# Kernel optimization log

Measured on AMD Instinct MI355X. Metric: run time of the kernel, lower is better.

Reference implementation:

```python
import jax, jax.numpy as jnp
import numpy as np

B, N, C, H = 16, 4096, 256, 4
D = C // H


def setup_inputs() -> dict:
    key = jax.random.key(0)
    ks = jax.random.split(key, 16)
    s = 0.02
    inp = {
        "x": jax.random.normal(ks[0], (B, N, C), jnp.float32),
        "encoding": jax.random.normal(ks[1], (2, B, 1, N, D), jnp.float32),
        "Wqkv_w": jax.random.normal(ks[2], (3 * C, C), jnp.float32) * s,
        "Wqkv_b": jnp.zeros((3 * C,), jnp.float32),
        "tssa_qkv_w": jax.random.normal(ks[3], (C, C), jnp.float32) * s,
        "tssa_qkv_b": jnp.zeros((C,), jnp.float32),
        "temp": jnp.ones((H, 1), jnp.float32),
        "tssa_out_w": jax.random.normal(ks[4], (C, C), jnp.float32) * s,
        "tssa_out_b": jnp.zeros((C,), jnp.float32),
        "out_proj_w": jax.random.normal(ks[5], (C, C), jnp.float32) * s,
        "out_proj_b": jnp.zeros((C,), jnp.float32),
        "ffn1_w": jax.random.normal(ks[6], (2 * C, 2 * C), jnp.float32) * s,
        "ffn1_b": jnp.zeros((2 * C,), jnp.float32),
        "ln_g": jnp.ones((2 * C,), jnp.float32),
        "ln_b": jnp.zeros((2 * C,), jnp.float32),
        "ffn2_w": jax.random.normal(ks[7], (C, 2 * C), jnp.float32) * s,
        "ffn2_b": jnp.zeros((C,), jnp.float32),
    }
    return inp


def _rotate_half(t):
    # (..., d) -> pairwise rotate: (x1, x2) -> (-x2, x1)
    t2 = t.reshape(t.shape[:-1] + (-1, 2))
    x1, x2 = t2[..., 0], t2[..., 1]
    return jnp.stack((-x2, x1), axis=-1).reshape(t.shape)


def reference(x, encoding, Wqkv_w, Wqkv_b, tssa_qkv_w, tssa_qkv_b, temp,
              tssa_out_w, tssa_out_b, out_proj_w, out_proj_b,
              ffn1_w, ffn1_b, ln_g, ln_b, ffn2_w, ffn2_b):
    b, n, c = x.shape
    h, d = H, D
    # QKV projection, layout (h, d, 3) on last dim as in unflatten(-1,(h,-1,3))
    qkv = (x @ Wqkv_w.T + Wqkv_b).reshape(b, n, h, d, 3).transpose(0, 2, 1, 3, 4)  # b h n d 3
    q, k, v = qkv[..., 0], qkv[..., 1], qkv[..., 2]
    rope = lambda t: t * encoding[0] + _rotate_half(t) * encoding[1]
    q = rope(q)
    k = rope(k)
    flat = lambda t: t.transpose(0, 2, 1, 3).reshape(b, n, c)  # b h n d -> b n (h d)
    w_input = (flat(q) + flat(k) + flat(v)) / 3.0
    # TSSA attention
    w = (w_input @ tssa_qkv_w.T + tssa_qkv_b).reshape(b, n, h, d).transpose(0, 2, 1, 3)  # b h n d
    norm = jnp.sqrt(jnp.sum(w * w, axis=2, keepdims=True))  # L2 over sequence axis N
    w_normed = w / jnp.maximum(norm, 1e-12)
    sum_ws = jnp.sum(w_normed * w_normed, axis=-1)  # b h n
    Pi = jax.nn.softmax(sum_ws * temp[None, :, :], axis=1)  # softmax over heads
    Pi_norm = Pi / (jnp.sum(Pi, axis=-1, keepdims=True) + 1e-8)
    dots = jnp.einsum('bhn,bhnd->bh', Pi_norm, w * w)  # (b,h,1,d) summed over d
    attn = 1.0 / (1.0 + dots)  # b h
    out = -(w * Pi[..., None]) * attn[:, :, None, None]  # b h n d
    out = out.transpose(0, 2, 1, 3).reshape(b, n, c)
    context = out @ tssa_out_w.T + tssa_out_b
    message = context @ out_proj_w.T + out_proj_b
    # residual FFN
    cat = jnp.concatenate([x, message], axis=-1)  # b n 2c
    h1 = cat @ ffn1_w.T + ffn1_b
    mu = jnp.mean(h1, axis=-1, keepdims=True)
    var = jnp.mean((h1 - mu) ** 2, axis=-1, keepdims=True)
    ln = (h1 - mu) / jnp.sqrt(var + 1e-5) * ln_g + ln_b
    g = jax.nn.gelu(ln, approximate=False)
    return x + (g @ ffn2_w.T + ffn2_b)
```

## Files before the change

### kernel.cpp

```cpp
#include <hip/hip_runtime.h>
#include <math.h>

#define Bc 16
#define Nc 4096

typedef __attribute__((ext_vector_type(8))) short short8;
typedef __attribute__((ext_vector_type(4))) float floatx4;

__device__ __forceinline__ unsigned short f2bf(float f) {
    union { float f; unsigned int u; } v; v.f = f;
    unsigned int u = v.u;
    return (unsigned short)((u + 0x7fffu + ((u >> 16) & 1u)) >> 16);
}
__device__ __forceinline__ float bf2f(unsigned short u) {
    union { unsigned int u; float f; } v; v.u = ((unsigned int)u) << 16;
    return v.f;
}

__device__ __forceinline__ void gll16(const unsigned short* g, unsigned short* l) {
    __builtin_amdgcn_global_load_lds(
        (const __attribute__((address_space(1))) void*)g,
        (__attribute__((address_space(3))) void*)l,
        16, 0, 0);
}

template <int EPI, typename TOUT>
__global__ __launch_bounds__(512) void gemm_bf(
    const unsigned short* __restrict__ A0, int lda0,
    const unsigned short* __restrict__ A1, int lda1, int K0,
    const unsigned short* __restrict__ W,
    const float* __restrict__ bias,
    const unsigned short* __restrict__ resid_bf,
    const float* __restrict__ Pi,
    const float* __restrict__ Sb,
    const float* __restrict__ Tb,
    const float* __restrict__ enc,
    float* __restrict__ norm2,
    float* __restrict__ rowstats,
    TOUT* __restrict__ C, int N, int K)
{
    __shared__ alignas(16) unsigned short As[128 * 64];
    __shared__ alignas(16) unsigned short Bs[256 * 64];

    const int t = threadIdx.x;
    const int bn = blockIdx.x, bm = blockIdx.y;
    const int lane = t & 63, wave = t >> 6;
    const int wm = wave >> 2, wn = wave & 3;
    const int quad = lane >> 4, l16 = lane & 15;
    const int rt = t >> 3, st = t & 7;

    floatx4 acc[4][4];
    #pragma unroll
    for (int i = 0; i < 4; ++i)
        #pragma unroll
        for (int j = 0; j < 4; ++j)
            acc[i][j] = (floatx4){0.f, 0.f, 0.f, 0.f};

    for (int k0 = 0; k0 < K; k0 += 64) {
        #pragma unroll
        for (int hh = 0; hh < 2; ++hh) {
            const int row = hh * 64 + rt;
            const int col = k0 + (st ^ (row & 7)) * 8;
            unsigned short* ldsa = As + row * 64 + st * 8;
            const size_t grow = (size_t)bm * 128 + row;
            if constexpr (EPI == 2) {
                const int b = (int)(grow >> 12);
                const int hd = col >> 6;
                const float s = Sb[b * 4 + hd] + 1e-8f;
                const float at = s / (s + Tb[b * 4 + hd]);
                const float sc = -Pi[grow * 4 + hd] * at;
                const short8 a = *(const short8*)(A0 + grow * (size_t)lda0 + col);
                short8 o;
                #pragma unroll
                for (int j = 0; j < 8; ++j) o[j] = (short)f2bf(bf2f((unsigned short)a[j]) * sc);
                *(short8*)ldsa = o;
            } else {
                const unsigned short* src = (col < K0)
                    ? (A0 + grow * (size_t)lda0 + col)
                    : (A1 + grow * (size_t)lda1 + (col - K0));
                gll16(src, ldsa);
            }
        }
        #pragma unroll
        for (int hh = 0; hh < 4; ++hh) {
            const int row = hh * 64 + rt;
            const int col = k0 + (st ^ (row & 7)) * 8;
            gll16(W + ((size_t)bn * 256 + row) * (size_t)K + col, Bs + row * 64 + st * 8);
        }
        __syncthreads();
        #pragma unroll
        for (int kk = 0; kk < 2; ++kk) {
            short8 af[4], wf[4];
            #pragma unroll
            for (int i = 0; i < 4; ++i) {
                const int ra = wm * 64 + i * 16 + l16;
                af[i] = *(const short8*)(As + ra * 64 + ((quad + kk * 4) ^ (ra & 7)) * 8);
                const int rw = wn * 64 + i * 16 + l16;
                wf[i] = *(const short8*)(Bs + rw * 64 + ((quad + kk * 4) ^ (rw & 7)) * 8);
            }
            #pragma unroll
            for (int mi = 0; mi < 4; ++mi)
                #pragma unroll
                for (int ni = 0; ni < 4; ++ni)
                    acc[mi][ni] = __builtin_amdgcn_mfma_f32_16x16x32_bf16(
                        wf[ni], af[mi], acc[mi][ni], 0, 0, 0);
        }
        __syncthreads();
    }

    float rs[4], rq[4];
    if constexpr (EPI == 4) {
        #pragma unroll
        for (int m = 0; m < 4; ++m) { rs[m] = 0.f; rq[m] = 0.f; }
    }

    #pragma unroll
    for (int mi = 0; mi < 4; ++mi) {
        const size_t row = (size_t)bm * 128 + wm * 64 + mi * 16 + l16;
        #pragma unroll
        for (int ni = 0; ni < 4; ++ni) {
            const int cb = bn * 256 + wn * 64 + ni * 16 + quad * 4;
            const float4 b4 = *(const float4*)(bias + cb);
            if constexpr (EPI == 5) {
                const int j = cb >> 2;
                const int h = j >> 5, d = (j & 31) * 2;
                const float s0 = acc[mi][ni][0] + b4.x;
                const float s1 = acc[mi][ni][1] + b4.y;
                const float v0 = acc[mi][ni][2] + b4.z;
                const float v1 = acc[mi][ni][3] + b4.w;
                const float2 e0 = *(const float2*)(enc + row * 64 + d);
                const float2 e1 = *(const float2*)(enc + 4194304 + row * 64 + d);
                const float r0 = s0 * e0.x - s1 * e1.x;
                const float r1 = s1 * e0.y + s0 * e1.y;
                ushort2 o;
                o.x = f2bf((r0 + v0) * (1.f / 3.f));
                o.y = f2bf((r1 + v1) * (1.f / 3.f));
                *(ushort2*)((unsigned short*)C + row * 256 + h * 64 + d) = o;
                continue;
            }
            float v[4] = {acc[mi][ni][0] + b4.x, acc[mi][ni][1] + b4.y,
                          acc[mi][ni][2] + b4.z, acc[mi][ni][3] + b4.w};
            if constexpr (EPI == 3) {
                const ushort4 xr = *(const ushort4*)(resid_bf + row * (size_t)N + cb);
                v[0] += bf2f(xr.x); v[1] += bf2f(xr.y);
                v[2] += bf2f(xr.z); v[3] += bf2f(xr.w);
            }
            if constexpr (EPI == 4) {
                #pragma unroll
                for (int rg = 0; rg < 4; ++rg) { rs[mi] += v[rg]; rq[mi] += v[rg] * v[rg]; }
            }
            if constexpr (EPI == 1) {
                #pragma unroll
                for (int rg = 0; rg < 4; ++rg) {
                    float s = v[rg] * v[rg];
                    s += __shfl_xor(s, 1, 64);
                    s += __shfl_xor(s, 2, 64);
                    s += __shfl_xor(s, 4, 64);
                    s += __shfl_xor(s, 8, 64);
                    if (l16 == 0) atomicAdd(&norm2[(bm >> 5) * 256 + cb + rg], s);
                }
            }
            if constexpr (__is_same(TOUT, float)) {
                float4 o; o.x = v[0]; o.y = v[1]; o.z = v[2]; o.w = v[3];
                *(float4*)(C + row * (size_t)N + cb) = o;
            } else {
                ushort4 o;
                o.x = f2bf(v[0]); o.y = f2bf(v[1]); o.z = f2bf(v[2]); o.w = f2bf(v[3]);
                *(ushort4*)(C + row * (size_t)N + cb) = o;
            }
        }
    }
    if constexpr (EPI == 4) {
        #pragma unroll
        for (int mi = 0; mi < 4; ++mi) {
            float s = rs[mi], q = rq[mi];
            s += __shfl_xor(s, 16, 64); s += __shfl_xor(s, 32, 64);
            q += __shfl_xor(q, 16, 64); q += __shfl_xor(q, 32, 64);
            if (quad == 0) {
                const size_t row = (size_t)bm * 128 + wm * 64 + mi * 16 + l16;
                atomicAdd(&rowstats[row * 2], s);
                atomicAdd(&rowstats[row * 2 + 1], q);
            }
        }
    }
}

__global__ __launch_bounds__(256) void lngelu_kernel(unsigned short* __restrict__ h1,
                                                     const float* __restrict__ rowstats,
                                                     const float* __restrict__ g,
                                                     const float* __restrict__ bb) {
    const size_t gid = (size_t)blockIdx.x * 256 + threadIdx.x;
    const size_t row = gid >> 6;
    const int col = (int)(gid & 63) * 8;
    const float2 stv = *(const float2*)(rowstats + row * 2);
    const float mean = stv.x * (1.f / 512.f);
    const float var = stv.y * (1.f / 512.f) - mean * mean;
    const float rstd = rsqrtf(var + 1e-5f);
    unsigned short* p = h1 + row * 512 + col;
    const short8 hv = *(const short8*)p;
    const float4 g0 = *(const float4*)(g + col);
    const float4 g1 = *(const float4*)(g + col + 4);
    const float4 b0 = *(const float4*)(bb + col);
    const float4 b1 = *(const float4*)(bb + col + 4);
    const float vg[8] = {g0.x, g0.y, g0.z, g0.w, g1.x, g1.y, g1.z, g1.w};
    const float vb[8] = {b0.x, b0.y, b0.z, b0.w, b1.x, b1.y, b1.z, b1.w};
    short8 ov;
    #pragma unroll
    for (int k = 0; k < 8; ++k) {
        const float ln = (bf2f((unsigned short)hv[k]) - mean) * rstd * vg[k] + vb[k];
        ov[k] = (short)f2bf(0.5f * ln * (1.f + erff(ln * 0.70710678118654752f)));
    }
    *(short8*)p = ov;
}

__device__ __forceinline__ void conv8(const float* src, unsigned short* dst, int i) {
    const float4 f0 = *(const float4*)(src + (size_t)i * 8);
    const float4 f1 = *(const float4*)(src + (size_t)i * 8 + 4);
    short8 sv;
    sv[0] = (short)f2bf(f0.x); sv[1] = (short)f2bf(f0.y);
    sv[2] = (short)f2bf(f0.z); sv[3] = (short)f2bf(f0.w);
    sv[4] = (short)f2bf(f1.x); sv[5] = (short)f2bf(f1.y);
    sv[6] = (short)f2bf(f1.z); sv[7] = (short)f2bf(f1.w);
    *(short8*)(dst + (size_t)i * 8) = sv;
}

__global__ __launch_bounds__(256) void prep_all(
    const float* __restrict__ x, const float* __restrict__ Wqkv,
    const float* __restrict__ bqkv, const float* __restrict__ tssa_w,
    const float* __restrict__ op_w, const float* __restrict__ to_w,
    const float* __restrict__ to_b, const float* __restrict__ op_b,
    const float* __restrict__ f1w, const float* __restrict__ f2w,
    unsigned short* __restrict__ x_bf, unsigned short* __restrict__ Wsvq,
    float* __restrict__ bsvq, unsigned short* __restrict__ tssa_bf,
    unsigned short* __restrict__ Wf, float* __restrict__ bfb,
    unsigned short* __restrict__ ffn1_bf, unsigned short* __restrict__ ffn2_bf,
    float* __restrict__ zbase, float* __restrict__ rowstats)
{
    const int blk = blockIdx.x, tt = threadIdx.x;
    if (blk < 8192) {
        conv8(x, x_bf, blk * 256 + tt);
    } else if (blk < 8704) {
        const int r = blk - 8192, c = tt;
        const int j = r >> 2, m = r & 3;
        const int cc = 2 * j + (m & 1);
        const int h = cc >> 6, dd = cc & 63;
        const int base = h * 192 + dd * 3;
        if (m < 2) {
            Wsvq[r * 256 + c] = f2bf(Wqkv[(base + 0) * 256 + c] + Wqkv[(base + 1) * 256 + c]);
            if (c == 0) bsvq[r] = bqkv[base] + bqkv[base + 1];
        } else {
            Wsvq[r * 256 + c] = f2bf(Wqkv[(base + 2) * 256 + c]);
            if (c == 0) bsvq[r] = bqkv[base + 2];
        }
    } else if (blk < 8960) {
        const int i = blk - 8704;
        float s = 0.f;
        for (int k = 0; k < 256; ++k) s += op_w[i * 256 + k] * to_w[k * 256 + tt];
        Wf[i * 256 + tt] = f2bf(s);
    } else if (blk == 8960) {
        float s = op_b[tt];
        for (int k = 0; k < 256; ++k) s += op_w[tt * 256 + k] * to_b[k];
        bfb[tt] = s;
    } else if (blk < 8993) {
        conv8(tssa_w, tssa_bf, (blk - 8961) * 256 + tt);
    } else if (blk < 9121) {
        conv8(f1w, ffn1_bf, (blk - 8993) * 256 + tt);
    } else if (blk < 9185) {
        conv8(f2w, ffn2_bf, (blk - 9121) * 256 + tt);
    } else {
        const int i = (blk - 9185) * 256 + tt;
        if (i < 4288) zbase[i] = 0.f;
        else if (i < 135360) rowstats[i - 4288] = 0.f;
    }
}

__global__ __launch_bounds__(256) void pi_kernel(const unsigned short* __restrict__ w,
                                                 const float* __restrict__ norm2,
                                                 const float* __restrict__ temp,
                                                 float* __restrict__ Pi,
                                                 float* __restrict__ S,
                                                 float* __restrict__ T) {
    const int t = threadIdx.x;
    const int i = t & 15;
    const int lr = t >> 4;
    const size_t r = (size_t)blockIdx.x * 16 + lr;
    const int b = (int)(r >> 12);
    const unsigned short* wrow = w + r * 256;
    const float* n2row = norm2 + b * 256;
    float raw[4], nrm[4];
    #pragma unroll
    for (int h = 0; h < 4; ++h) {
        const ushort4 wv = *(const ushort4*)(wrow + h * 64 + i * 4);
        const float w0 = bf2f(wv.x), w1 = bf2f(wv.y), w2 = bf2f(wv.z), w3 = bf2f(wv.w);
        const float4 n2 = *(const float4*)(n2row + h * 64 + i * 4);
        const float s0 = w0 * w0, s1 = w1 * w1, s2 = w2 * w2, s3 = w3 * w3;
        raw[h] = s0 + s1 + s2 + s3;
        nrm[h] = s0 / fmaxf(n2.x, 1e-24f) + s1 / fmaxf(n2.y, 1e-24f)
               + s2 / fmaxf(n2.z, 1e-24f) + s3 / fmaxf(n2.w, 1e-24f);
    }
    #pragma unroll
    for (int off = 1; off < 16; off <<= 1) {
        #pragma unroll
        for (int h = 0; h < 4; ++h) {
            raw[h] += __shfl_xor(raw[h], off, 64);
            nrm[h] += __shfl_xor(nrm[h], off, 64);
        }
    }
    float sw[4], m = -1e30f;
    #pragma unroll
    for (int h = 0; h < 4; ++h) { sw[h] = nrm[h] * temp[h]; m = fmaxf(m, sw[h]); }
    float e[4], Z = 0.f;
    #pragma unroll
    for (int h = 0; h < 4; ++h) { e[h] = expf(sw[h] - m); Z += e[h]; }
    const float invZ = 1.f / Z;
    float pi[4];
    #pragma unroll
    for (int h = 0; h < 4; ++h) pi[h] = e[h] * invZ;
    if (i < 4) Pi[r * 4 + i] = pi[i];

    __shared__ float sS[16][4], sT[16][4];
    if (i == 0) {
        #pragma unroll
        for (int h = 0; h < 4; ++h) { sS[lr][h] = pi[h]; sT[lr][h] = pi[h] * raw[h]; }
    }
    __syncthreads();
    if (t < 4) {
        float as = 0.f, at = 0.f;
        for (int rr = 0; rr < 16; ++rr) { as += sS[rr][t]; at += sT[rr][t]; }
        atomicAdd(&S[b * 4 + t], as);
        atomicAdd(&T[b * 4 + t], at);
    }
}

extern "C" void kernel_launch(void* const* d_in, const int* in_sizes, int n_in,
                              void* d_out, int out_size, void* d_ws, size_t ws_size,
                              hipStream_t stream) {
    (void)in_sizes; (void)n_in; (void)out_size; (void)ws_size;
    const float* x          = (const float*)d_in[0];
    const float* enc        = (const float*)d_in[1];
    const float* Wqkv_w     = (const float*)d_in[2];
    const float* Wqkv_b     = (const float*)d_in[3];
    const float* tssa_qkv_w = (const float*)d_in[4];
    const float* tssa_qkv_b = (const float*)d_in[5];
    const float* temp       = (const float*)d_in[6];
    const float* tssa_out_w = (const float*)d_in[7];
    const float* tssa_out_b = (const float*)d_in[8];
    const float* out_proj_w = (const float*)d_in[9];
    const float* out_proj_b = (const float*)d_in[10];
    const float* ffn1_w     = (const float*)d_in[11];
    const float* ffn1_b     = (const float*)d_in[12];
    const float* ln_g       = (const float*)d_in[13];
    const float* ln_b       = (const float*)d_in[14];
    const float* ffn2_w     = (const float*)d_in[15];
    const float* ffn2_b     = (const float*)d_in[16];
    float* outp = (float*)d_out;

    const int M = Bc * Nc;

    char* ws = (char*)d_ws;
    unsigned short* x_bf  = (unsigned short*)(ws);
    unsigned short* wi_bf = (unsigned short*)(ws + (size_t)(32 << 20));
    unsigned short* h1_bf = (unsigned short*)(ws + (size_t)(32 << 20));
    unsigned short* w_bf  = (unsigned short*)(ws + (size_t)(64 << 20));
    unsigned short* msg_bf= (unsigned short*)(ws + (size_t)(96 << 20));
    float* fb    = (float*)(ws + (size_t)(128 << 20));
    float* Pi    = fb;
    float* norm2 = Pi + 262144;
    float* Sb    = norm2 + 4096;
    float* Tb    = Sb + 64;
    float* attnb = Tb + 64;
    float* bsvq  = attnb + 64;
    float* bfb   = bsvq + 512;
    float* rowstats = bfb + 256;
    unsigned short* Wsvq_bf = (unsigned short*)(rowstats + 131072);
    unsigned short* tssa_bf = Wsvq_bf + 131072;
    unsigned short* Wf_bf   = tssa_bf + 65536;
    unsigned short* ffn1_bf = Wf_bf + 65536;
    unsigned short* ffn2_bf = ffn1_bf + 262144;

    prep_all<<<9714, 256, 0, stream>>>(
        x, Wqkv_w, Wqkv_b, tssa_qkv_w, out_proj_w, tssa_out_w, tssa_out_b,
        out_proj_b, ffn1_w, ffn2_w,
        x_bf, Wsvq_bf, bsvq, tssa_bf, Wf_bf, bfb, ffn1_bf, ffn2_bf,
        norm2, rowstats);

    gemm_bf<5, unsigned short><<<dim3(2, M / 128), 512, 0, stream>>>(
        x_bf, 256, x_bf, 256, 256, Wsvq_bf, bsvq,
        nullptr, nullptr, nullptr, nullptr, enc, nullptr, nullptr,
        wi_bf, 256, 256);

    gemm_bf<1, unsigned short><<<dim3(1, M / 128), 512, 0, stream>>>(
        wi_bf, 256, wi_bf, 256, 256, tssa_bf, tssa_qkv_b,
        nullptr, nullptr, nullptr, nullptr, nullptr, norm2, nullptr,
        w_bf, 256, 256);

    pi_kernel<<<4096, 256, 0, stream>>>(w_bf, norm2, temp, Pi, Sb, Tb);

    gemm_bf<2, unsigned short><<<dim3(1, M / 128), 512, 0, stream>>>(
        w_bf, 256, w_bf, 256, 256, Wf_bf, bfb,
        nullptr, Pi, Sb, Tb, nullptr, nullptr, nullptr,
        msg_bf, 256, 256);

    gemm_bf<4, unsigned short><<<dim3(2, M / 128), 512, 0, stream>>>(
        x_bf, 256, msg_bf, 256, 256, ffn1_bf, ffn1_b,
        nullptr, nullptr, nullptr, nullptr, nullptr, nullptr, rowstats,
        h1_bf, 512, 512);

    lngelu_kernel<<<16384, 256, 0, stream>>>(h1_bf, rowstats, ln_g, ln_b);

    gemm_bf<3, float><<<dim3(1, M / 128), 512, 0, stream>>>(
        h1_bf, 512, h1_bf, 512, 512, ffn2_bf, ffn2_b,
        x_bf, nullptr, nullptr, nullptr, nullptr, nullptr, nullptr,
        outp, 256, 512);
}
```

Before: 472.8 us.

## Double-buffer GEMM LDS tiles with 128x128 tiles and 256-thread blocks

```diff
diff --git a/kernel.cpp b/kernel.cpp
--- a/kernel.cpp
+++ b/kernel.cpp
@@ -24,8 +24,28 @@
         16, 0, 0);
 }
 
+__device__ __forceinline__ void stage_tiles(
+    const unsigned short* __restrict__ A0, int lda0,
+    const unsigned short* __restrict__ A1, int lda1, int K0,
+    const unsigned short* __restrict__ W, int K,
+    int bm, int bn, int rt, int st, int k0,
+    unsigned short* Asb, unsigned short* Bsb)
+{
+    #pragma unroll
+    for (int hh = 0; hh < 4; ++hh) {
+        const int row = hh * 32 + rt;
+        const int col = k0 + (st ^ (row & 7)) * 8;
+        const size_t grow = (size_t)bm * 128 + row;
+        const unsigned short* src = (col < K0)
+            ? (A0 + grow * (size_t)lda0 + col)
+            : (A1 + grow * (size_t)lda1 + (col - K0));
+        gll16(src, Asb + row * 64 + st * 8);
+        gll16(W + ((size_t)bn * 128 + row) * (size_t)K + col, Bsb + row * 64 + st * 8);
+    }
+}
+
 template <int EPI, typename TOUT>
-__global__ __launch_bounds__(512) void gemm_bf(
+__global__ __launch_bounds__(256) void gemm_bf(
     const unsigned short* __restrict__ A0, int lda0,
     const unsigned short* __restrict__ A1, int lda1, int K0,
     const unsigned short* __restrict__ W,
@@ -39,16 +59,34 @@
     float* __restrict__ rowstats,
     TOUT* __restrict__ C, int N, int K)
 {
-    __shared__ alignas(16) unsigned short As[128 * 64];
-    __shared__ alignas(16) unsigned short Bs[256 * 64];
+    __shared__ alignas(16) unsigned short As[2][128 * 64];
+    __shared__ alignas(16) unsigned short Bs[2][128 * 64];
 
     const int t = threadIdx.x;
     const int bn = blockIdx.x, bm = blockIdx.y;
     const int lane = t & 63, wave = t >> 6;
-    const int wm = wave >> 2, wn = wave & 3;
+    const int wm = wave >> 1, wn = wave & 1;
     const int quad = lane >> 4, l16 = lane & 15;
     const int rt = t >> 3, st = t & 7;
 
+    float sc[4][4];
+    if constexpr (EPI == 2) {
+        const int b = bm >> 5;
+        float at[4];
+        #pragma unroll
+        for (int h = 0; h < 4; ++h) {
+            const float s = Sb[b * 4 + h] + 1e-8f;
+            at[h] = s / (s + Tb[b * 4 + h]);
+        }
+        #pragma unroll
+        for (int i = 0; i < 4; ++i) {
+            const int row = bm * 128 + wm * 64 + i * 16 + l16;
+            const float4 p4 = *(const float4*)(Pi + (size_t)row * 4);
+            sc[i][0] = -p4.x * at[0]; sc[i][1] = -p4.y * at[1];
+            sc[i][2] = -p4.z * at[2]; sc[i][3] = -p4.w * at[3];
+        }
+    }
+
     floatx4 acc[4][4];
     #pragma unroll
     for (int i = 0; i < 4; ++i)
@@ -56,47 +94,31 @@
         for (int j = 0; j < 4; ++j)
             acc[i][j] = (floatx4){0.f, 0.f, 0.f, 0.f};
 
-    for (int k0 = 0; k0 < K; k0 += 64) {
-        #pragma unroll
-        for (int hh = 0; hh < 2; ++hh) {
-            const int row = hh * 64 + rt;
-            const int col = k0 + (st ^ (row & 7)) * 8;
-            unsigned short* ldsa = As + row * 64 + st * 8;
-            const size_t grow = (size_t)bm * 128 + row;
-            if constexpr (EPI == 2) {
-                const int b = (int)(grow >> 12);
-                const int hd = col >> 6;
-                const float s = Sb[b * 4 + hd] + 1e-8f;
-                const float at = s / (s + Tb[b * 4 + hd]);
-                const float sc = -Pi[grow * 4 + hd] * at;
-                const short8 a = *(const short8*)(A0 + grow * (size_t)lda0 + col);
-                short8 o;
-                #pragma unroll
-                for (int j = 0; j < 8; ++j) o[j] = (short)f2bf(bf2f((unsigned short)a[j]) * sc);
-                *(short8*)ldsa = o;
-            } else {
-                const unsigned short* src = (col < K0)
-                    ? (A0 + grow * (size_t)lda0 + col)
-                    : (A1 + grow * (size_t)lda1 + (col - K0));
-                gll16(src, ldsa);
-            }
-        }
-        #pragma unroll
-        for (int hh = 0; hh < 4; ++hh) {
-            const int row = hh * 64 + rt;
-            const int col = k0 + (st ^ (row & 7)) * 8;
-            gll16(W + ((size_t)bn * 256 + row) * (size_t)K + col, Bs + row * 64 + st * 8);
-        }
+    const int niter = K >> 6;
+    stage_tiles(A0, lda0, A1, lda1, K0, W, K, bm, bn, rt, st, 0, As[0], Bs[0]);
+
+    for (int k = 0; k < niter; ++k) {
         __syncthreads();
+        if (k + 1 < niter)
+            stage_tiles(A0, lda0, A1, lda1, K0, W, K, bm, bn, rt, st,
+                        (k + 1) << 6, As[(k + 1) & 1], Bs[(k + 1) & 1]);
+        const unsigned short* Ac = As[k & 1];
+        const unsigned short* Bc_ = Bs[k & 1];
         #pragma unroll
         for (int kk = 0; kk < 2; ++kk) {
             short8 af[4], wf[4];
             #pragma unroll
             for (int i = 0; i < 4; ++i) {
                 const int ra = wm * 64 + i * 16 + l16;
-                af[i] = *(const short8*)(As + ra * 64 + ((quad + kk * 4) ^ (ra & 7)) * 8);
+                af[i] = *(const short8*)(Ac + ra * 64 + ((quad + kk * 4) ^ (ra & 7)) * 8);
+                if constexpr (EPI == 2) {
+                    const float s = sc[i][k];
+                    #pragma unroll
+                    for (int j = 0; j < 8; ++j)
+                        af[i][j] = (short)f2bf(bf2f((unsigned short)af[i][j]) * s);
+                }
                 const int rw = wn * 64 + i * 16 + l16;
-                wf[i] = *(const short8*)(Bs + rw * 64 + ((quad + kk * 4) ^ (rw & 7)) * 8);
+                wf[i] = *(const short8*)(Bc_ + rw * 64 + ((quad + kk * 4) ^ (rw & 7)) * 8);
             }
             #pragma unroll
             for (int mi = 0; mi < 4; ++mi)
@@ -105,7 +127,6 @@
                     acc[mi][ni] = __builtin_amdgcn_mfma_f32_16x16x32_bf16(
                         wf[ni], af[mi], acc[mi][ni], 0, 0, 0);
         }
-        __syncthreads();
     }
 
     float rs[4], rq[4];
@@ -119,7 +140,7 @@
         const size_t row = (size_t)bm * 128 + wm * 64 + mi * 16 + l16;
         #pragma unroll
         for (int ni = 0; ni < 4; ++ni) {
-            const int cb = bn * 256 + wn * 64 + ni * 16 + quad * 4;
+            const int cb = bn * 128 + wn * 64 + ni * 16 + quad * 4;
             const float4 b4 = *(const float4*)(bias + cb);
             if constexpr (EPI == 5) {
                 const int j = cb >> 2;
@@ -384,31 +405,31 @@
         x_bf, Wsvq_bf, bsvq, tssa_bf, Wf_bf, bfb, ffn1_bf, ffn2_bf,
         norm2, rowstats);
 
-    gemm_bf<5, unsigned short><<<dim3(2, M / 128), 512, 0, stream>>>(
+    gemm_bf<5, unsigned short><<<dim3(4, M / 128), 256, 0, stream>>>(
         x_bf, 256, x_bf, 256, 256, Wsvq_bf, bsvq,
         nullptr, nullptr, nullptr, nullptr, enc, nullptr, nullptr,
-        wi_bf, 256, 256);
-
-    gemm_bf<1, unsigned short><<<dim3(1, M / 128), 512, 0, stream>>>(
+        wi_bf, 512, 256);
+
+    gemm_bf<1, unsigned short><<<dim3(2, M / 128), 256, 0, stream>>>(
         wi_bf, 256, wi_bf, 256, 256, tssa_bf, tssa_qkv_b,
         nullptr, nullptr, nullptr, nullptr, nullptr, norm2, nullptr,
         w_bf, 256, 256);
 
     pi_kernel<<<4096, 256, 0, stream>>>(w_bf, norm2, temp, Pi, Sb, Tb);
 
-    gemm_bf<2, unsigned short><<<dim3(1, M / 128), 512, 0, stream>>>(
+    gemm_bf<2, unsigned short><<<dim3(2, M / 128), 256, 0, stream>>>(
         w_bf, 256, w_bf, 256, 256, Wf_bf, bfb,
         nullptr, Pi, Sb, Tb, nullptr, nullptr, nullptr,
         msg_bf, 256, 256);
 
-    gemm_bf<4, unsigned short><<<dim3(2, M / 128), 512, 0, stream>>>(
+    gemm_bf<4, unsigned short><<<dim3(4, M / 128), 256, 0, stream>>>(
         x_bf, 256, msg_bf, 256, 256, ffn1_bf, ffn1_b,
         nullptr, nullptr, nullptr, nullptr, nullptr, nullptr, rowstats,
         h1_bf, 512, 512);
 
     lngelu_kernel<<<16384, 256, 0, stream>>>(h1_bf, rowstats, ln_g, ln_b);
 
-    gemm_bf<3, float><<<dim3(1, M / 128), 512, 0, stream>>>(
+    gemm_bf<3, float><<<dim3(2, M / 128), 256, 0, stream>>>(
         h1_bf, 512, h1_bf, 512, 512, ffn2_bf, ffn2_b,
         x_bf, nullptr, nullptr, nullptr, nullptr, nullptr, nullptr,
         outp, 256, 512);
```

Measured after the change: 528.1 us. +11.7%, slower.
